# Performance work log

Measured on AMD Instinct MI355X. Metric: run time of the kernel, lower is better.

Reference implementation:

```python
import jax, jax.numpy as jnp
import numpy as np

NUM_TRAIN = 256  # num_train_anchors
N, A, T = 8, 131072, 64


def _make_boxes(key, shape2):
    # shape2 = (..., 2) of (y, x); returns valid boxes (y1, x1, y2, x2) in [0, 1]
    k1, k2 = jax.random.split(key)
    c1 = jax.random.uniform(k1, shape2, dtype=jnp.float32)
    c2 = jax.random.uniform(k2, shape2, dtype=jnp.float32)
    lo = jnp.minimum(c1, c2)
    hi = jnp.maximum(c1, c2)
    return jnp.stack([lo[..., 0], lo[..., 1], hi[..., 0], hi[..., 1]], axis=-1)


def setup_inputs() -> dict:
    key = jax.random.key(0)
    ka, kt, kp, kn = jax.random.split(key, 4)
    return {
        "anchors": _make_boxes(ka, (N, A, 2)),
        "true_bboxes": _make_boxes(kt, (N, T, 2)),
        "rand_pos": jax.random.uniform(kp, (N, A), dtype=jnp.float32),
        "rand_neg": jax.random.uniform(kn, (N, A), dtype=jnp.float32),
    }


def _bbox_overlap(anchors, gt):
    # anchors [A,4], gt [T,4] -> IoU [A,T]
    ay1, ax1, ay2, ax2 = [anchors[:, i] for i in range(4)]
    gy1, gx1, gy2, gx2 = [gt[:, i] for i in range(4)]
    a_area = (ay2 - ay1) * (ax2 - ax1)                       # [A]
    g_area = (gy2 - gy1) * (gx2 - gx1)                       # [T]
    ih = jnp.clip(jnp.minimum(ay2[:, None], gy2[None, :]) - jnp.maximum(ay1[:, None], gy1[None, :]), 0.0)
    iw = jnp.clip(jnp.minimum(ax2[:, None], gx2[None, :]) - jnp.maximum(ax1[:, None], gx1[None, :]), 0.0)
    inter = ih * iw                                          # [A,T]
    union = a_area[:, None] + g_area[None, :] - inter
    return jnp.where(union > 0, inter / jnp.where(union > 0, union, 1.0), 0.0)


def _rank_of(scores):
    # rank[i] = position of element i in ascending sort of scores
    order = jnp.argsort(scores)
    return jnp.zeros(scores.shape[0], jnp.int32).at[order].set(jnp.arange(scores.shape[0], dtype=jnp.int32))


def _compute_bbox_deltas(anchors, gt):
    # standard (dy, dx, dh, dw) encoding with safe denominators
    ah = anchors[:, 2] - anchors[:, 0]
    aw = anchors[:, 3] - anchors[:, 1]
    acy = anchors[:, 0] + 0.5 * ah
    acx = anchors[:, 1] + 0.5 * aw
    gh = gt[:, 2] - gt[:, 0]
    gw = gt[:, 3] - gt[:, 1]
    gcy = gt[:, 0] + 0.5 * gh
    gcx = gt[:, 1] + 0.5 * gw
    ah_s = jnp.where(ah > 0, ah, 1.0)
    aw_s = jnp.where(aw > 0, aw, 1.0)
    gh_s = jnp.where(gh > 0, gh, 1.0)
    gw_s = jnp.where(gw > 0, gw, 1.0)
    return jnp.stack([(gcy - acy) / ah_s, (gcx - acx) / aw_s,
                      jnp.log(gh_s / ah_s), jnp.log(gw_s / aw_s)], axis=-1)


def _get_targets(anchors, gt, r_pos, r_neg):
    na = anchors.shape[0]
    # strip_out_of_bounds_anchors: zero out anchors falling outside [0,1]^2 (keeps static shape)
    inb = (anchors[:, 0] >= 0) & (anchors[:, 1] >= 0) & (anchors[:, 2] <= 1) & (anchors[:, 3] <= 1)
    anchors = jnp.where(inb[:, None], anchors, 0.0)

    overlaps = _bbox_overlap(anchors, gt)                    # [A,T]

    # --- class assignment ---
    iou_max_val = jnp.max(overlaps, axis=1)                  # [A]
    classes = jnp.full((na,), -1, jnp.int32)
    classes = jnp.where(iou_max_val < 0.3, 0, classes)
    iou_max_anchor = jnp.argmax(overlaps, axis=0)            # [T] best anchor per gt
    pos_anchor = jnp.zeros((na,), jnp.int32).at[iou_max_anchor].set(1)
    classes = jnp.where(pos_anchor > 0, 1, classes)
    classes = jnp.where(iou_max_val >= 0.7, 1, classes)

    # --- subsample positives to NUM_TRAIN//2 (uniform random subset) ---
    pos = classes > 0
    rank_p = _rank_of(jnp.where(pos, r_pos, jnp.inf))
    keep_pos = pos & (rank_p < NUM_TRAIN // 2)
    classes = jnp.where(pos & ~keep_pos, -1, classes)
    n_pos = jnp.sum(keep_pos.astype(jnp.int32))

    # --- subsample negatives to NUM_TRAIN - n_pos ---
    desired_neg = NUM_TRAIN - n_pos
    neg = classes == 0
    rank_n = _rank_of(jnp.where(neg, r_neg, jnp.inf))
    keep_neg = neg & (rank_n < desired_neg)
    classes = jnp.where(neg & ~keep_neg, -1, classes)

    # --- deltas for positive anchors ---
    best_gt = jnp.argmax(overlaps, axis=1)                   # [A]
    deltas = _compute_bbox_deltas(anchors, gt[best_gt])      # [A,4]
    deltas = jnp.where((classes > 0)[:, None], deltas, 0.0)
    return classes, deltas


def reference(anchors, true_bboxes, rand_pos, rand_neg):
    classes, deltas = jax.vmap(_get_targets)(anchors, true_bboxes, rand_pos, rand_neg)
    return classes, deltas
```

## Files before the change

kernel.cpp:

```cpp
#include <hip/hip_runtime.h>
#include <stdint.h>

#define N_B 8
#define A_N 131072
#define T_N 64
#define NUM_TRAIN 256
#define NEG_TAU 0.05f
#define ITEM_CAP 512
#define HSET 512
#define APT 2
#define SEG_A 512
#define GBLK_A 256
#define CAPP 128
#define BLK_C 128
#define SEG_C 1024

typedef unsigned long long u64;
typedef unsigned int u32;

__device__ __forceinline__ float iou_one(float ay1, float ax1, float ay2, float ax2,
                                         float a_area, float gy1, float gx1, float gy2,
                                         float gx2, float g_area) {
#pragma clang fp contract(off)
    float ih = fmaxf(fminf(ay2, gy2) - fmaxf(ay1, gy1), 0.0f);
    float iw = fmaxf(fminf(ax2, gx2) - fmaxf(ax1, gx1), 0.0f);
    float inter = ih * iw;
    float uni = (a_area + g_area) - inter;
    return uni > 0.0f ? inter / uni : 0.0f;
}

__global__ void __launch_bounds__(256) k_main(const float4* __restrict__ anchors4,
                                              const float4* __restrict__ gts4,
                                              const float* __restrict__ rpos,
                                              const float* __restrict__ rneg,
                                              unsigned char* __restrict__ preclass,
                                              long long* __restrict__ colpack,
                                              u64* __restrict__ pos_list,
                                              u64* __restrict__ neg_list,
                                              int* __restrict__ bcp, int* __restrict__ bcn) {
    __shared__ float4 gbox[T_N];
    __shared__ float gars[T_N];
    __shared__ u64 cmax[T_N];
    __shared__ int lcnt[2];
    int n = blockIdx.y, bx = blockIdx.x, tid = threadIdx.x, lane = tid & 63;
    int a0 = bx * SEG_A + tid;
    size_t nA = (size_t)n * A_N;

    if (tid < T_N) {
        float4 gb = gts4[n * T_N + tid];
        gbox[tid] = gb;
        {
#pragma clang fp contract(off)
            gars[tid] = (gb.z - gb.x) * (gb.w - gb.y);
        }
        cmax[tid] = 0;
    }
    if (tid < 2) lcnt[tid] = 0;
    __syncthreads();

    float ay1[APT], ax1[APT], ay2[APT], ax2[APT], aar[APT], vmax[APT];
#pragma unroll
    for (int k = 0; k < APT; k++) {
        float4 ab = anchors4[nA + a0 + k * 256];
        float y1 = ab.x, x1 = ab.y, y2 = ab.z, x2 = ab.w;
        bool inb = (y1 >= 0.f) && (x1 >= 0.f) && (y2 <= 1.f) && (x2 <= 1.f);
        if (!inb) { y1 = x1 = y2 = x2 = 0.f; }
        ay1[k] = y1; ax1[k] = x1; ay2[k] = y2; ax2[k] = x2;
        {
#pragma clang fp contract(off)
            aar[k] = (y2 - y1) * (x2 - x1);
        }
        vmax[k] = 0.f;
    }

#pragma unroll 4
    for (int jj = 0; jj < T_N; jj++) {
        int j = (lane + jj) & (T_N - 1);
        float4 gb = gbox[j];
        float gar = gars[j];
        float vb = iou_one(ay1[0], ax1[0], ay2[0], ax2[0], aar[0], gb.x, gb.y, gb.z, gb.w, gar);
        vmax[0] = fmaxf(vmax[0], vb);
        int kb = 0;
#pragma unroll
        for (int k = 1; k < APT; k++) {
            float v = iou_one(ay1[k], ax1[k], ay2[k], ax2[k], aar[k], gb.x, gb.y, gb.z, gb.w, gar);
            vmax[k] = fmaxf(vmax[k], v);
            if (v > vb) { vb = v; kb = k; }
        }
        u64 pk = ((u64)__float_as_uint(vb) << 32) | (u32)(~(u32)(a0 + (kb << 8)));
        atomicMax(&cmax[j], pk);
    }

    size_t segbase = ((size_t)(n * GBLK_A + bx)) << 7;
#pragma unroll
    for (int k = 0; k < APT; k++) {
        int a = a0 + k * 256;
        float vm = vmax[k];
        int c0 = (vm < 0.3f) ? 0 : ((vm >= 0.7f) ? 1 : -1);
        preclass[nA + a] = (unsigned char)(signed char)c0;
        if (c0 == 1) {
            int sl = atomicAdd(&lcnt[0], 1);
            if (sl < CAPP)
                pos_list[segbase + sl] = ((u64)__float_as_uint(rpos[nA + a]) << 32) | (u32)a;
        } else if (c0 == 0) {
            float r = rneg[nA + a];
            if (r < NEG_TAU) {
                int sl = atomicAdd(&lcnt[1], 1);
                if (sl < CAPP)
                    neg_list[segbase + sl] = ((u64)__float_as_uint(r) << 32) | (u32)a;
            }
        }
    }
    __syncthreads();
    if (tid < T_N) atomicMax(&colpack[(n << 6) + tid], (long long)cmax[tid]);
    if (tid == 0) {
        bcp[n * GBLK_A + bx] = lcnt[0] < CAPP ? lcnt[0] : CAPP;
        bcn[n * GBLK_A + bx] = lcnt[1] < CAPP ? lcnt[1] : CAPP;
    }
}

__device__ __forceinline__ bool in_hset(const int* hset, int a) {
    u32 h = ((u32)a * 2654435761u) >> 23 & (HSET - 1);
    while (true) {
        int v = hset[h];
        if (v == -1) return false;
        if (v == a) return true;
        h = (h + 1) & (HSET - 1);
    }
}

__device__ u64 select_kth2(const u64* lists, const int* scnt,
                           const u64* extras, int ecnt, const int* hset, bool use_excl,
                           int k, float scale, u64 ovf_all,
                           int* hist, u64* items, int* misc, int* wsum, u64* result) {
    int tid = threadIdx.x, lane = tid & 63, wid = tid >> 6;
    hist[tid] = 0;
    if (tid == 0) { misc[0] = 0; *result = ovf_all; }
    __syncthreads();

    int c = scnt[tid];
    const ulonglong2* b2 = (const ulonglong2*)(lists + ((size_t)tid << 7));
    int nch = (c + 1) >> 1;

    {
        ulonglong2 q;
        if (nch > 0) q = b2[0];
        for (int ci = 0; ci < nch; ci++) {
            ulonglong2 qn;
            if (ci + 1 < nch) qn = b2[ci + 1];
            {
                u64 p = q.x; int a = (int)(u32)p;
                if (!use_excl || !in_hset(hset, a)) {
                    float v = __uint_as_float((u32)(p >> 32));
                    int bb = (int)(v * scale); bb = bb > 255 ? 255 : bb;
                    atomicAdd(&hist[bb], 1);
                }
            }
            if (2 * ci + 1 < c) {
                u64 p = q.y; int a = (int)(u32)p;
                if (!use_excl || !in_hset(hset, a)) {
                    float v = __uint_as_float((u32)(p >> 32));
                    int bb = (int)(v * scale); bb = bb > 255 ? 255 : bb;
                    atomicAdd(&hist[bb], 1);
                }
            }
            q = qn;
        }
    }
    for (int i = tid; i < ecnt; i += 256) {
        float v = __uint_as_float((u32)(extras[i] >> 32));
        int bb = (int)(v * scale); bb = bb > 255 ? 255 : bb;
        atomicAdd(&hist[bb], 1);
    }
    __syncthreads();

    int h = hist[tid], v = h;
#pragma unroll
    for (int d = 1; d < 64; d <<= 1) {
        int t = __shfl_up(v, d, 64);
        if (lane >= d) v += t;
    }
    if (lane == 63) wsum[wid] = v;
    __syncthreads();
    int base = 0;
    for (int w = 0; w < wid; w++) base += wsum[w];
    int total = wsum[0] + wsum[1] + wsum[2] + wsum[3];
    int incl = base + v, exc = incl - h;
    if (k >= exc && k < incl) { misc[1] = tid; misc[2] = exc; }
    __syncthreads();
    if (k >= total) return ovf_all;
    int b = misc[1], before = misc[2];

    {
        ulonglong2 q;
        if (nch > 0) q = b2[0];
        for (int ci = 0; ci < nch; ci++) {
            ulonglong2 qn;
            if (ci + 1 < nch) qn = b2[ci + 1];
            {
                u64 p = q.x; int a = (int)(u32)p;
                if (!use_excl || !in_hset(hset, a)) {
                    float vv = __uint_as_float((u32)(p >> 32));
                    int bn = (int)(vv * scale); bn = bn > 255 ? 255 : bn;
                    if (bn == b) { int ix = atomicAdd(&misc[0], 1); if (ix < ITEM_CAP) items[ix] = p; }
                }
            }
            if (2 * ci + 1 < c) {
                u64 p = q.y; int a = (int)(u32)p;
                if (!use_excl || !in_hset(hset, a)) {
                    float vv = __uint_as_float((u32)(p >> 32));
                    int bn = (int)(vv * scale); bn = bn > 255 ? 255 : bn;
                    if (bn == b) { int ix = atomicAdd(&misc[0], 1); if (ix < ITEM_CAP) items[ix] = p; }
                }
            }
            q = qn;
        }
    }
    for (int i = tid; i < ecnt; i += 256) {
        u64 p = extras[i];
        float vv = __uint_as_float((u32)(p >> 32));
        int bn = (int)(vv * scale); bn = bn > 255 ? 255 : bn;
        if (bn == b) { int ix = atomicAdd(&misc[0], 1); if (ix < ITEM_CAP) items[ix] = p; }
    }
    __syncthreads();
    int m = misc[0]; m = m < ITEM_CAP ? m : ITEM_CAP;
    int target = k - before;
    for (int i = tid; i < m; i += 256) {
        u64 p = items[i];
        int r = 0;
        for (int j = 0; j < m; j++) r += (items[j] < p);
        if (r == target) *result = p;
    }
    __syncthreads();
    u64 res = *result;
    __syncthreads();
    return res;
}

__global__ void __launch_bounds__(256) k_B(const u64* __restrict__ pos_list,
                                           const u64* __restrict__ neg_list,
                                           const int* __restrict__ bcp,
                                           const int* __restrict__ bcn,
                                           const long long* __restrict__ colpack,
                                           const unsigned char* __restrict__ preclass,
                                           const float* __restrict__ rpos,
                                           int* __restrict__ wnr_g,
                                           u64* __restrict__ cutoff) {
    __shared__ int sbp[GBLK_A], sbn[GBLK_A];
    __shared__ int wnrs[T_N];
    __shared__ u64 extras[T_N];
    __shared__ int hist[256];
    __shared__ u64 items[ITEM_CAP];
    __shared__ int hset[HSET];
    __shared__ int misc[4];
    __shared__ int wsum[4];
    __shared__ int shr[10];
    __shared__ u64 result;
    int n = blockIdx.y, role = blockIdx.x, tid = threadIdx.x, lane = tid & 63, wid = tid >> 6;
    size_t nA = (size_t)n * A_N;

    int pv = bcp[n * GBLK_A + tid];
    sbp[tid] = pv;
    sbn[tid] = bcn[n * GBLK_A + tid];
#pragma unroll
    for (int off = 32; off > 0; off >>= 1) pv += __shfl_xor(pv, off, 64);
    if (lane == 0) shr[wid] = pv;

    for (int i = tid; i < HSET; i += 256) hset[i] = -1;
    __syncthreads();

    if (tid < T_N) {
        u64 m = (u64)colpack[(n << 6) + tid];
        int w = (int)(~(u32)(m & 0xFFFFFFFFull));
        wnrs[tid] = w;
        if (role == 0) wnr_g[n * T_N + tid] = w;
        u32 hh = ((u32)w * 2654435761u) >> 23 & (HSET - 1);
        while (true) {
            int old = atomicCAS(&hset[hh], -1, w);
            if (old == -1 || old == w) break;
            hh = (hh + 1) & (HSET - 1);
        }
    }
    __syncthreads();
    if (tid < T_N) {
        int w = wnrs[tid];
        bool dup = false;
        for (int t2 = 0; t2 < tid; t2++) dup |= (wnrs[t2] == w);
        int pc = (int)(signed char)preclass[nA + w];
        bool val = !dup && (pc != 1);
        u64 mask = __ballot(val);
        if (role == 0 && val) {
            int ix = (int)__popcll(mask & ((1ull << lane) - 1));
            extras[ix] = ((u64)__float_as_uint(rpos[nA + w]) << 32) | (u32)w;
        }
        if (tid == 0) shr[8] = (int)__popcll(mask);
    }
    __syncthreads();
    int extra_cnt = shr[8];
    int P = shr[0] + shr[1] + shr[2] + shr[3] + extra_cnt;

    if (role == 0) {
        u64 cpos = ~0ull;
        if (NUM_TRAIN / 2 < P)
            cpos = select_kth2(pos_list + (((size_t)n * GBLK_A) << 7), sbp,
                               extras, extra_cnt, hset, false,
                               NUM_TRAIN / 2, 256.0f, ~0ull,
                               hist, items, misc, wsum, &result);
        if (tid == 0) cutoff[2 * n] = cpos;
    } else {
        int n_pos = P < NUM_TRAIN / 2 ? P : NUM_TRAIN / 2;
        int k_neg = NUM_TRAIN - n_pos;
        u64 cneg = select_kth2(neg_list + (((size_t)n * GBLK_A) << 7), sbn,
                               nullptr, 0, hset, true,
                               k_neg, 256.0f / NEG_TAU, ((u64)__float_as_uint(NEG_TAU) << 32),
                               hist, items, misc, wsum, &result);
        if (tid == 0) cutoff[2 * n + 1] = cneg;
    }
}

__global__ void __launch_bounds__(256) k_C(const float4* __restrict__ anchors4,
                                           const float4* __restrict__ gts4,
                                           const u32* __restrict__ preclass32,
                                           const int* __restrict__ wnr_g,
                                           const float4* __restrict__ rpos4,
                                           const float4* __restrict__ rneg4,
                                           const u64* __restrict__ cutoff,
                                           float4* __restrict__ out_classes4,
                                           float4* __restrict__ out_deltas) {
    __shared__ float4 gbox[T_N];
    __shared__ float gars[T_N];
    __shared__ u32 wbm[32];
    int n = blockIdx.y, bx = blockIdx.x, tid = threadIdx.x;
    size_t nA = (size_t)n * A_N;
    if (tid < 32) wbm[tid] = 0;
    __syncthreads();
    if (tid < T_N) {
        float4 gb = gts4[n * T_N + tid];
        gbox[tid] = gb;
        {
#pragma clang fp contract(off)
            gars[tid] = (gb.z - gb.x) * (gb.w - gb.y);
        }
        int w = wnr_g[n * T_N + tid];
        int d = w - bx * SEG_C;
        if ((u32)d < (u32)SEG_C) atomicOr(&wbm[d >> 5], 1u << (d & 31));
    }
    __syncthreads();

    size_t gi4 = nA / 4 + bx * 256 + tid;
    u32 pcw = preclass32[gi4];
    float4 rp = rpos4[gi4];
    float4 rn = rneg4[gi4];
    float rpv[4] = {rp.x, rp.y, rp.z, rp.w};
    float rnv[4] = {rn.x, rn.y, rn.z, rn.w};
    int a0 = (bx * 256 + tid) * 4;
    u64 cp = cutoff[2 * n], cn = cutoff[2 * n + 1];

    u32 marked = (wbm[tid >> 3] >> ((tid & 7) * 4)) & 0xF;

    float fcv[4];
#pragma unroll
    for (int j = 0; j < 4; j++) {
        int c = (int)(signed char)((pcw >> (8 * j)) & 0xFF);
        if ((marked >> j) & 1) c = 1;
        int a = a0 + j;
        int fc = -1;
        if (c == 1) {
            u64 p = ((u64)__float_as_uint(rpv[j]) << 32) | (u32)a;
            fc = (p < cp) ? 1 : -1;
        } else if (c == 0) {
            u64 p = ((u64)__float_as_uint(rnv[j]) << 32) | (u32)a;
            fc = (p < cn) ? 0 : -1;
        }
        fcv[j] = (float)fc;

        float4 d = make_float4(0.f, 0.f, 0.f, 0.f);
        if (fc == 1) {
            float4 ab = anchors4[nA + a];
            float ay1 = ab.x, ax1 = ab.y, ay2 = ab.z, ax2 = ab.w;
            bool inb = (ay1 >= 0.f) && (ax1 >= 0.f) && (ay2 <= 1.f) && (ax2 <= 1.f);
            if (!inb) { ay1 = ax1 = ay2 = ax2 = 0.f; }
            float a_area;
            {
#pragma clang fp contract(off)
                a_area = (ay2 - ay1) * (ax2 - ax1);
            }
            float vm = 0.f; int jb = 0;
            for (int t = 0; t < T_N; t++) {
                float4 gb = gbox[t];
                float v = iou_one(ay1, ax1, ay2, ax2, a_area, gb.x, gb.y, gb.z, gb.w, gars[t]);
                bool g = v > vm;
                vm = g ? v : vm;
                jb = g ? t : jb;
            }
            float4 gb = gbox[jb];
            float ah = ay2 - ay1, aw = ax2 - ax1;
            float acy = ay1 + 0.5f * ah, acx = ax1 + 0.5f * aw;
            float gh = gb.z - gb.x, gw = gb.w - gb.y;
            float gcy = gb.x + 0.5f * gh, gcx = gb.y + 0.5f * gw;
            float ah_s = ah > 0.f ? ah : 1.f, aw_s = aw > 0.f ? aw : 1.f;
            float gh_s = gh > 0.f ? gh : 1.f, gw_s = gw > 0.f ? gw : 1.f;
            d.x = (gcy - acy) / ah_s;
            d.y = (gcx - acx) / aw_s;
            d.z = logf(gh_s / ah_s);
            d.w = logf(gw_s / aw_s);
        }
        out_deltas[nA + a] = d;
    }
    out_classes4[gi4] = make_float4(fcv[0], fcv[1], fcv[2], fcv[3]);
}

extern "C" void kernel_launch(void* const* d_in, const int* in_sizes, int n_in,
                              void* d_out, int out_size, void* d_ws, size_t ws_size,
                              hipStream_t stream) {
    const float4* anchors4 = (const float4*)d_in[0];
    const float4* gts4     = (const float4*)d_in[1];
    const float*  rpos     = (const float*)d_in[2];
    const float*  rneg     = (const float*)d_in[3];

    char* p = (char*)d_ws;
    u64* cutoff   = (u64*)p;  p += 2 * N_B * sizeof(u64);
    long long* colpack = (long long*)p; p += N_B * T_N * sizeof(long long);
    u64* pos_list = (u64*)p;  p += (size_t)N_B * GBLK_A * CAPP * sizeof(u64);
    u64* neg_list = (u64*)p;  p += (size_t)N_B * GBLK_A * CAPP * sizeof(u64);
    unsigned char* preclass = (unsigned char*)p; p += (size_t)N_B * A_N;
    int* bcp  = (int*)p;  p += N_B * GBLK_A * sizeof(int);
    int* bcn  = (int*)p;  p += N_B * GBLK_A * sizeof(int);
    int* wnr  = (int*)p;  p += N_B * T_N * sizeof(int);

    float4* out_classes4 = (float4*)d_out;
    float4* out_deltas   = (float4*)((float*)d_out + (size_t)N_B * A_N);

    k_main<<<dim3(GBLK_A, N_B), 256, 0, stream>>>(anchors4, gts4, rpos, rneg, preclass,
                                                  colpack, pos_list, neg_list, bcp, bcn);
    k_B<<<dim3(2, N_B), 256, 0, stream>>>(pos_list, neg_list, bcp, bcn, colpack,
                                          preclass, rpos, wnr, cutoff);
    k_C<<<dim3(BLK_C, N_B), 256, 0, stream>>>(anchors4, gts4, (const u32*)preclass, wnr,
                                              (const float4*)rpos, (const float4*)rneg,
                                              cutoff, out_classes4, out_deltas);
}
```

Before: 173.5 us.

## Build selection histograms in main kernel and widen selection kernel to 1024 threads

Builds the positive and negative random-value histograms during the main IoU kernel with global atomics, so the selection kernel no longer does a full histogram pass over the candidate lists. The selection kernel grows from 256 to 1024 threads, which split the second pass (bin gathering) across segments. Exclusions for forced-positive anchors are handled by decrementing the negative histogram. This adds global atomics in the main kernel and a memset launch, and it removes the early skip when positives number at most the target.

New measurement: 169.9 us. 1.02x faster.

```diff
diff --git a/kernel.cpp b/kernel.cpp
--- a/kernel.cpp
+++ b/kernel.cpp
@@ -12,6 +12,7 @@
 #define SEG_A 512
 #define GBLK_A 256
 #define CAPP 128
+#define KB_THREADS 1024
 #define BLK_C 128
 #define SEG_C 1024
 
@@ -37,7 +38,9 @@
                                               long long* __restrict__ colpack,
                                               u64* __restrict__ pos_list,
                                               u64* __restrict__ neg_list,
-                                              int* __restrict__ bcp, int* __restrict__ bcn) {
+                                              int* __restrict__ bcp, int* __restrict__ bcn,
+                                              int* __restrict__ hist_pos,
+                                              int* __restrict__ hist_neg) {
     __shared__ float4 gbox[T_N];
     __shared__ float gars[T_N];
     __shared__ u64 cmax[T_N];
@@ -100,14 +103,21 @@
         preclass[nA + a] = (unsigned char)(signed char)c0;
         if (c0 == 1) {
             int sl = atomicAdd(&lcnt[0], 1);
-            if (sl < CAPP)
-                pos_list[segbase + sl] = ((u64)__float_as_uint(rpos[nA + a]) << 32) | (u32)a;
+            if (sl < CAPP) {
+                float r = rpos[nA + a];
+                pos_list[segbase + sl] = ((u64)__float_as_uint(r) << 32) | (u32)a;
+                int bb = (int)(r * 256.0f); bb = bb > 255 ? 255 : bb;
+                atomicAdd(&hist_pos[(n << 8) + bb], 1);
+            }
         } else if (c0 == 0) {
             float r = rneg[nA + a];
             if (r < NEG_TAU) {
                 int sl = atomicAdd(&lcnt[1], 1);
-                if (sl < CAPP)
+                if (sl < CAPP) {
                     neg_list[segbase + sl] = ((u64)__float_as_uint(r) << 32) | (u32)a;
+                    int bb = (int)(r * (256.0f / NEG_TAU)); bb = bb > 255 ? 255 : bb;
+                    atomicAdd(&hist_neg[(n << 8) + bb], 1);
+                }
             }
         }
     }
@@ -129,94 +139,58 @@
     }
 }
 
-__device__ u64 select_kth2(const u64* lists, const int* scnt,
-                           const u64* extras, int ecnt, const int* hset, bool use_excl,
-                           int k, float scale, u64 ovf_all,
-                           int* hist, u64* items, int* misc, int* wsum, u64* result) {
+__device__ u64 select_from_hist(const u64* lists, const int* cnts,
+                                const u64* extras, int ecnt, const int* hset, bool use_excl,
+                                int k, float scale, u64 ovf_all,
+                                int* hist, u64* items, int* misc, int* wsum, u64* result) {
     int tid = threadIdx.x, lane = tid & 63, wid = tid >> 6;
-    hist[tid] = 0;
     if (tid == 0) { misc[0] = 0; *result = ovf_all; }
     __syncthreads();
 
-    int c = scnt[tid];
-    const ulonglong2* b2 = (const ulonglong2*)(lists + ((size_t)tid << 7));
-    int nch = (c + 1) >> 1;
-
-    {
-        ulonglong2 q;
-        if (nch > 0) q = b2[0];
-        for (int ci = 0; ci < nch; ci++) {
-            ulonglong2 qn;
-            if (ci + 1 < nch) qn = b2[ci + 1];
-            {
-                u64 p = q.x; int a = (int)(u32)p;
-                if (!use_excl || !in_hset(hset, a)) {
-                    float v = __uint_as_float((u32)(p >> 32));
-                    int bb = (int)(v * scale); bb = bb > 255 ? 255 : bb;
-                    atomicAdd(&hist[bb], 1);
-                }
-            }
-            if (2 * ci + 1 < c) {
-                u64 p = q.y; int a = (int)(u32)p;
-                if (!use_excl || !in_hset(hset, a)) {
-                    float v = __uint_as_float((u32)(p >> 32));
-                    int bb = (int)(v * scale); bb = bb > 255 ? 255 : bb;
-                    atomicAdd(&hist[bb], 1);
-                }
-            }
-            q = qn;
-        }
-    }
-    for (int i = tid; i < ecnt; i += 256) {
-        float v = __uint_as_float((u32)(extras[i] >> 32));
-        int bb = (int)(v * scale); bb = bb > 255 ? 255 : bb;
-        atomicAdd(&hist[bb], 1);
-    }
-    __syncthreads();
-
-    int h = hist[tid], v = h;
+    int h = 0, v = 0;
+    if (tid < 256) { h = hist[tid]; v = h; }
 #pragma unroll
     for (int d = 1; d < 64; d <<= 1) {
         int t = __shfl_up(v, d, 64);
         if (lane >= d) v += t;
     }
-    if (lane == 63) wsum[wid] = v;
-    __syncthreads();
-    int base = 0;
-    for (int w = 0; w < wid; w++) base += wsum[w];
+    if (tid < 256 && lane == 63) wsum[wid] = v;
+    __syncthreads();
     int total = wsum[0] + wsum[1] + wsum[2] + wsum[3];
-    int incl = base + v, exc = incl - h;
-    if (k >= exc && k < incl) { misc[1] = tid; misc[2] = exc; }
+    if (tid < 256) {
+        int base = 0;
+        for (int w = 0; w < wid; w++) base += wsum[w];
+        int incl = base + v, exc = incl - h;
+        if (k >= exc && k < incl) { misc[1] = tid; misc[2] = exc; }
+    }
     __syncthreads();
     if (k >= total) return ovf_all;
     int b = misc[1], before = misc[2];
 
-    {
-        ulonglong2 q;
-        if (nch > 0) q = b2[0];
-        for (int ci = 0; ci < nch; ci++) {
-            ulonglong2 qn;
-            if (ci + 1 < nch) qn = b2[ci + 1];
-            {
-                u64 p = q.x; int a = (int)(u32)p;
-                if (!use_excl || !in_hset(hset, a)) {
-                    float vv = __uint_as_float((u32)(p >> 32));
-                    int bn = (int)(vv * scale); bn = bn > 255 ? 255 : bn;
-                    if (bn == b) { int ix = atomicAdd(&misc[0], 1); if (ix < ITEM_CAP) items[ix] = p; }
-                }
-            }
-            if (2 * ci + 1 < c) {
-                u64 p = q.y; int a = (int)(u32)p;
-                if (!use_excl || !in_hset(hset, a)) {
-                    float vv = __uint_as_float((u32)(p >> 32));
-                    int bn = (int)(vv * scale); bn = bn > 255 ? 255 : bn;
-                    if (bn == b) { int ix = atomicAdd(&misc[0], 1); if (ix < ITEM_CAP) items[ix] = p; }
-                }
-            }
-            q = qn;
-        }
-    }
-    for (int i = tid; i < ecnt; i += 256) {
+    int seg = tid & (GBLK_A - 1), part = tid >> 8;
+    int c = cnts[seg];
+    const ulonglong2* b2 = (const ulonglong2*)(lists + ((size_t)seg << 7));
+    int nch = (c + 1) >> 1;
+    for (int ci = part; ci < nch; ci += KB_THREADS / GBLK_A) {
+        ulonglong2 q = b2[ci];
+        {
+            u64 p = q.x; int a = (int)(u32)p;
+            if (!use_excl || !in_hset(hset, a)) {
+                float vv = __uint_as_float((u32)(p >> 32));
+                int bn = (int)(vv * scale); bn = bn > 255 ? 255 : bn;
+                if (bn == b) { int ix = atomicAdd(&misc[0], 1); if (ix < ITEM_CAP) items[ix] = p; }
+            }
+        }
+        if (2 * ci + 1 < c) {
+            u64 p = q.y; int a = (int)(u32)p;
+            if (!use_excl || !in_hset(hset, a)) {
+                float vv = __uint_as_float((u32)(p >> 32));
+                int bn = (int)(vv * scale); bn = bn > 255 ? 255 : bn;
+                if (bn == b) { int ix = atomicAdd(&misc[0], 1); if (ix < ITEM_CAP) items[ix] = p; }
+            }
+        }
+    }
+    for (int i = tid; i < ecnt; i += KB_THREADS) {
         u64 p = extras[i];
         float vv = __uint_as_float((u32)(p >> 32));
         int bn = (int)(vv * scale); bn = bn > 255 ? 255 : bn;
@@ -225,7 +199,7 @@
     __syncthreads();
     int m = misc[0]; m = m < ITEM_CAP ? m : ITEM_CAP;
     int target = k - before;
-    for (int i = tid; i < m; i += 256) {
+    for (int i = tid; i < m; i += KB_THREADS) {
         u64 p = items[i];
         int r = 0;
         for (int j = 0; j < m; j++) r += (items[j] < p);
@@ -237,16 +211,18 @@
     return res;
 }
 
-__global__ void __launch_bounds__(256) k_B(const u64* __restrict__ pos_list,
-                                           const u64* __restrict__ neg_list,
-                                           const int* __restrict__ bcp,
-                                           const int* __restrict__ bcn,
-                                           const long long* __restrict__ colpack,
-                                           const unsigned char* __restrict__ preclass,
-                                           const float* __restrict__ rpos,
-                                           int* __restrict__ wnr_g,
-                                           u64* __restrict__ cutoff) {
-    __shared__ int sbp[GBLK_A], sbn[GBLK_A];
+__global__ void __launch_bounds__(KB_THREADS) k_B(const u64* __restrict__ pos_list,
+                                                  const u64* __restrict__ neg_list,
+                                                  const int* __restrict__ bcp,
+                                                  const int* __restrict__ bcn,
+                                                  const long long* __restrict__ colpack,
+                                                  const unsigned char* __restrict__ preclass,
+                                                  const float* __restrict__ rpos,
+                                                  const float* __restrict__ rneg,
+                                                  const int* __restrict__ hist_pos_g,
+                                                  const int* __restrict__ hist_neg_g,
+                                                  int* __restrict__ wnr_g,
+                                                  u64* __restrict__ cutoff) {
     __shared__ int wnrs[T_N];
     __shared__ u64 extras[T_N];
     __shared__ int hist[256];
@@ -254,19 +230,14 @@
     __shared__ int hset[HSET];
     __shared__ int misc[4];
     __shared__ int wsum[4];
-    __shared__ int shr[10];
+    __shared__ int shr[4];
     __shared__ u64 result;
-    int n = blockIdx.y, role = blockIdx.x, tid = threadIdx.x, lane = tid & 63, wid = tid >> 6;
+    int n = blockIdx.y, role = blockIdx.x, tid = threadIdx.x, lane = tid & 63;
     size_t nA = (size_t)n * A_N;
 
-    int pv = bcp[n * GBLK_A + tid];
-    sbp[tid] = pv;
-    sbn[tid] = bcn[n * GBLK_A + tid];
-#pragma unroll
-    for (int off = 32; off > 0; off >>= 1) pv += __shfl_xor(pv, off, 64);
-    if (lane == 0) shr[wid] = pv;
-
-    for (int i = tid; i < HSET; i += 256) hset[i] = -1;
+    if (tid < 256) hist[tid] = (role == 0 ? hist_pos_g : hist_neg_g)[(n << 8) + tid];
+    if (tid == 0) shr[1] = 0;
+    for (int i = tid; i < HSET; i += KB_THREADS) hset[i] = -1;
     __syncthreads();
 
     if (tid < T_N) {
@@ -281,7 +252,14 @@
             hh = (hh + 1) & (HSET - 1);
         }
     }
-    __syncthreads();
+    if (role == 1) {
+        int pv = (tid < 256) ? hist_pos_g[(n << 8) + tid] : 0;
+#pragma unroll
+        for (int off = 32; off > 0; off >>= 1) pv += __shfl_xor(pv, off, 64);
+        if (lane == 0 && tid < 256) atomicAdd(&shr[1], pv);
+    }
+    __syncthreads();
+
     if (tid < T_N) {
         int w = wnrs[tid];
         bool dup = false;
@@ -293,27 +271,37 @@
             int ix = (int)__popcll(mask & ((1ull << lane) - 1));
             extras[ix] = ((u64)__float_as_uint(rpos[nA + w]) << 32) | (u32)w;
         }
-        if (tid == 0) shr[8] = (int)__popcll(mask);
-    }
-    __syncthreads();
-    int extra_cnt = shr[8];
-    int P = shr[0] + shr[1] + shr[2] + shr[3] + extra_cnt;
+        if (role == 1 && !dup && pc == 0) {
+            float r = rneg[nA + w];
+            if (r < NEG_TAU) {
+                int bb = (int)(r * (256.0f / NEG_TAU)); bb = bb > 255 ? 255 : bb;
+                atomicAdd(&hist[bb], -1);
+            }
+        }
+        if (tid == 0) shr[0] = (int)__popcll(mask);
+    }
+    __syncthreads();
+    int extra_cnt = shr[0];
 
     if (role == 0) {
-        u64 cpos = ~0ull;
-        if (NUM_TRAIN / 2 < P)
-            cpos = select_kth2(pos_list + (((size_t)n * GBLK_A) << 7), sbp,
-                               extras, extra_cnt, hset, false,
-                               NUM_TRAIN / 2, 256.0f, ~0ull,
-                               hist, items, misc, wsum, &result);
+        for (int i = tid; i < extra_cnt; i += KB_THREADS) {
+            float vv = __uint_as_float((u32)(extras[i] >> 32));
+            int bb = (int)(vv * 256.0f); bb = bb > 255 ? 255 : bb;
+            atomicAdd(&hist[bb], 1);
+        }
+        u64 cpos = select_from_hist(pos_list + (((size_t)n * GBLK_A) << 7), bcp + n * GBLK_A,
+                                    extras, extra_cnt, hset, false,
+                                    NUM_TRAIN / 2, 256.0f, ~0ull,
+                                    hist, items, misc, wsum, &result);
         if (tid == 0) cutoff[2 * n] = cpos;
     } else {
+        int P = shr[1] + extra_cnt;
         int n_pos = P < NUM_TRAIN / 2 ? P : NUM_TRAIN / 2;
         int k_neg = NUM_TRAIN - n_pos;
-        u64 cneg = select_kth2(neg_list + (((size_t)n * GBLK_A) << 7), sbn,
-                               nullptr, 0, hset, true,
-                               k_neg, 256.0f / NEG_TAU, ((u64)__float_as_uint(NEG_TAU) << 32),
-                               hist, items, misc, wsum, &result);
+        u64 cneg = select_from_hist(neg_list + (((size_t)n * GBLK_A) << 7), bcn + n * GBLK_A,
+                                    nullptr, 0, hset, true,
+                                    k_neg, 256.0f / NEG_TAU, ((u64)__float_as_uint(NEG_TAU) << 32),
+                                    hist, items, misc, wsum, &result);
         if (tid == 0) cutoff[2 * n + 1] = cneg;
     }
 }
@@ -427,14 +415,20 @@
     int* bcp  = (int*)p;  p += N_B * GBLK_A * sizeof(int);
     int* bcn  = (int*)p;  p += N_B * GBLK_A * sizeof(int);
     int* wnr  = (int*)p;  p += N_B * T_N * sizeof(int);
+    int* hist_pos_g = (int*)p; p += N_B * 256 * sizeof(int);
+    int* hist_neg_g = (int*)p; p += N_B * 256 * sizeof(int);
 
     float4* out_classes4 = (float4*)d_out;
     float4* out_deltas   = (float4*)((float*)d_out + (size_t)N_B * A_N);
 
+    hipMemsetAsync(hist_pos_g, 0, 2 * N_B * 256 * sizeof(int), stream);
+
     k_main<<<dim3(GBLK_A, N_B), 256, 0, stream>>>(anchors4, gts4, rpos, rneg, preclass,
-                                                  colpack, pos_list, neg_list, bcp, bcn);
-    k_B<<<dim3(2, N_B), 256, 0, stream>>>(pos_list, neg_list, bcp, bcn, colpack,
-                                          preclass, rpos, wnr, cutoff);
+                                                  colpack, pos_list, neg_list, bcp, bcn,
+                                                  hist_pos_g, hist_neg_g);
+    k_B<<<dim3(2, N_B), KB_THREADS, 0, stream>>>(pos_list, neg_list, bcp, bcn, colpack,
+                                                 preclass, rpos, rneg, hist_pos_g, hist_neg_g,
+                                                 wnr, cutoff);
     k_C<<<dim3(BLK_C, N_B), 256, 0, stream>>>(anchors4, gts4, (const u32*)preclass, wnr,
                                               (const float4*)rpos, (const float4*)rneg,
                                               cutoff, out_classes4, out_deltas);
```
